# Performance work log

Measured on AMD Instinct MI355X. Metric: run time of the kernel, lower is better.

The kernel has to match this reference:

```python
import jax, jax.numpy as jnp
import numpy as np

N, D, V = 262144, 3, 64
CAPACITY = 1 << 20  # hash table size (number of lattice vertices storable)
PRIMES = np.array([2654435761, 805459861, 3674653429], dtype=np.uint32)


def setup_inputs() -> dict:
    key = jax.random.key(0)
    k1, k2 = jax.random.split(key)
    positions = jax.random.normal(k1, (N, D), dtype=jnp.float32) * 2.0
    values = jax.random.normal(k2, (N, V), dtype=jnp.float32)
    return {"positions": positions, "values": values}


def _splat(positions, values):
    """Permutohedral-lattice splat: scatter-add barycentric-weighted homogeneous
    values into a hashed lattice table of shape [CAPACITY, V+1]."""
    n, d = positions.shape
    dp1 = d + 1
    # elevation scale factors (standard permutohedral construction)
    inv_std = np.sqrt(2.0 / 3.0) * dp1
    scale = (inv_std / np.sqrt((np.arange(d) + 1.0) * (np.arange(d) + 2.0))).astype(np.float32)
    cf = positions * scale                                   # [N, d]
    # elevated[i] = sum_{j>=i} cf_j - i * cf_{i-1}
    suf = jnp.cumsum(cf[:, ::-1], axis=1)[:, ::-1]           # suffix sums [N, d]
    suf_ext = jnp.concatenate([suf, jnp.zeros((n, 1), cf.dtype)], axis=1)  # [N, d+1]
    cf_pad = jnp.concatenate([jnp.zeros((n, 1), cf.dtype), cf], axis=1)
    i_arr = jnp.arange(dp1, dtype=cf.dtype)
    elev = suf_ext - i_arr * cf_pad                           # [N, d+1]

    # nearest 0-colored remainder point
    rd = jnp.round(elev / dp1)
    rem0 = rd * dp1                                           # [N, d+1]
    rd_sum = jnp.sum(rd, axis=1).astype(jnp.int32)            # [N]

    # rank: sort order of (elev - rem0), ties broken by index
    diff = elev - rem0
    dj = diff[:, :, None]
    di = diff[:, None, :]
    jidx = jnp.arange(dp1)[:, None]
    iidx = jnp.arange(dp1)[None, :]
    rank = jnp.sum(((dj > di) | ((dj == di) & (jidx < iidx))).astype(jnp.int32), axis=1)
    rank = rank + rd_sum[:, None]
    under = rank < 0
    over = rank > d
    rank = rank + jnp.where(under, dp1, 0) - jnp.where(over, dp1, 0)
    rem0 = rem0 + (under.astype(cf.dtype) - over.astype(cf.dtype)) * dp1

    # barycentric weights (length d+2, last entry folded into bary[0])
    delta = (elev - rem0) / dp1                               # [N, d+1]
    oh = (jax.nn.one_hot(d - rank, d + 2, dtype=cf.dtype)
          - jax.nn.one_hot(d + 1 - rank, d + 2, dtype=cf.dtype))  # [N, d+1, d+2]
    bary = jnp.einsum('nik,ni->nk', oh, delta)
    bary = bary.at[:, 0].add(1.0 + bary[:, d + 1])
    w = bary[:, :dp1]                                         # [N, d+1] simplex weights

    # simplex vertex keys per remainder r (only first d coords needed)
    r_arr = jnp.arange(dp1, dtype=jnp.int32)                  # [d+1]
    r_b = r_arr[None, :, None]                                # [1, d+1, 1]
    offs = jnp.where(rank[:, None, :d] < dp1 - r_b, r_b, r_b - dp1)  # [N, d+1, d]
    keys = rem0[:, None, :d].astype(jnp.int32) + offs         # [N, d+1, d]

    # hash keys into table slots
    h = (keys.astype(jnp.uint32) * jnp.asarray(PRIMES)).sum(-1) % jnp.uint32(CAPACITY)
    h = h.astype(jnp.int32)                                   # [N, d+1]

    # scatter-add weighted homogeneous values
    vh = jnp.concatenate([values, jnp.ones((n, 1), values.dtype)], axis=1)  # [N, V+1]
    contrib = w[:, :, None] * vh[:, None, :]                  # [N, d+1, V+1]
    table = jnp.zeros((CAPACITY, vh.shape[1]), values.dtype)
    table = table.at[h.reshape(-1)].add(contrib.reshape(-1, vh.shape[1]))
    return table


def reference(positions, values):
    return _splat(positions, values)
```

## Files before the change

### kernel.cpp

```cpp
#include <hip/hip_runtime.h>
#include <stdint.h>


#define CAPACITY (1u << 20)
#define KCAP     (1u << 20)
#define TBL_W 65
#define CHUNK 64

__device__ __forceinline__ void lattice_all(const float* __restrict__ pos, int point,
                                            uint32_t h[4], float w[4], uint32_t* keyOut)
{
    const float scale0 = 2.3094010767585034f;
    const float scale1 = 1.3333333333333333f;
    const float scale2 = 0.9428090415820634f;

    const float cf0 = pos[point * 3 + 0] * scale0;
    const float cf1 = pos[point * 3 + 1] * scale1;
    const float cf2 = pos[point * 3 + 2] * scale2;

    const float t1 = cf2 + cf1;
    float elev[4];
    elev[0] = t1 + cf0;
    elev[1] = t1 - cf0;
    elev[2] = cf2 - 2.0f * cf1;
    elev[3] = -3.0f * cf2;

    float rem0[4];
    float rd_s = 0.0f;
#pragma unroll
    for (int j = 0; j < 4; ++j) {
        float rd = rintf(elev[j] * 0.25f);
        rem0[j] = rd * 4.0f;
        rd_s += rd;
    }
    const int rd_sum = (int)rd_s;

    float diff[4];
#pragma unroll
    for (int j = 0; j < 4; ++j) diff[j] = elev[j] - rem0[j];

    int rank[4];
#pragma unroll
    for (int i = 0; i < 4; ++i) {
        int r = 0;
#pragma unroll
        for (int j = 0; j < 4; ++j) {
            if (diff[j] > diff[i] || (diff[j] == diff[i] && j < i)) r++;
        }
        rank[i] = r + rd_sum;
    }

#pragma unroll
    for (int i = 0; i < 4; ++i) {
        if (rank[i] < 0)      { rank[i] += 4; rem0[i] += 4.0f; }
        else if (rank[i] > 3) { rank[i] -= 4; rem0[i] -= 4.0f; }
    }

    float delta[4];
#pragma unroll
    for (int i = 0; i < 4; ++i) delta[i] = (elev[i] - rem0[i]) * 0.25f;

    float b[5] = {0.f, 0.f, 0.f, 0.f, 0.f};
#pragma unroll
    for (int i = 0; i < 4; ++i) {
        int k1 = 3 - rank[i];
        int k2 = 4 - rank[i];
        if (k1 >= 0 && k1 < 5) b[k1] += delta[i];
        if (k2 >= 0 && k2 < 5) b[k2] -= delta[i];
    }
    w[0] = b[0] + (1.0f + b[4]);
    w[1] = b[1];
    w[2] = b[2];
    w[3] = b[3];

    const uint32_t P0 = 2654435761u, P1 = 805459861u, P2 = 3674653429u;
    const int k0  = (int)rem0[0];
    const int k1i = (int)rem0[1];
    const int k2i = (int)rem0[2];

#pragma unroll
    for (int r = 0; r < 4; ++r) {
        int o0 = (rank[0] < 4 - r) ? r : r - 4;
        int o1 = (rank[1] < 4 - r) ? r : r - 4;
        int o2 = (rank[2] < 4 - r) ? r : r - 4;
        uint32_t hh = (uint32_t)(k0 + o0)  * P0
                    + (uint32_t)(k1i + o1) * P1
                    + (uint32_t)(k2i + o2) * P2;
        h[r] = hh & (CAPACITY - 1u);
    }

    const uint32_t pidx = (uint32_t)(rank[0] * 16 + rank[1] * 4 + rank[2]);
    uint32_t key = (uint32_t)k0 * P0 + (uint32_t)k1i * P1 + (uint32_t)k2i * P2
                 + pidx * 0x9E3779B9u;
    *keyOut = key & (KCAP - 1u);
}

__global__ __launch_bounds__(256) void k_hist(const float* __restrict__ pos,
                                              uint32_t* __restrict__ counts,
                                              uint32_t* __restrict__ keys, int n)
{
    int p = blockIdx.x * blockDim.x + threadIdx.x;
    if (p >= n) return;
    uint32_t h[4]; float w[4]; uint32_t key;
    lattice_all(pos, p, h, w, &key);
    keys[p] = key;
    atomicAdd(&counts[key], 1u);
}

__global__ __launch_bounds__(256) void k_blocksum(const uint32_t* __restrict__ counts,
                                                  uint32_t* __restrict__ partials)
{
    __shared__ uint32_t s[256];
    const int b = blockIdx.x, t = threadIdx.x;
    uint4 v = ((const uint4*)(counts + (size_t)b * 1024))[t];
    s[t] = v.x + v.y + v.z + v.w;
    __syncthreads();
    for (int o = 128; o > 0; o >>= 1) {
        if (t < o) s[t] += s[t + o];
        __syncthreads();
    }
    if (t == 0) partials[b] = s[0];
}

__global__ __launch_bounds__(1024) void k_scanpartials(uint32_t* __restrict__ partials,
                                                       int npart)
{
    __shared__ uint32_t s[1024];
    const int t = threadIdx.x;
    const int k = npart >> 10;
    uint32_t v[8];
    uint32_t tot = 0;
    for (int j = 0; j < k; ++j) { v[j] = partials[t * k + j]; tot += v[j]; }
    s[t] = tot;
    __syncthreads();
    for (int o = 1; o < 1024; o <<= 1) {
        uint32_t x = s[t];
        uint32_t y = (t >= o) ? s[t - o] : 0u;
        __syncthreads();
        s[t] = x + y;
        __syncthreads();
    }
    uint32_t run = (t > 0) ? s[t - 1] : 0u;
    for (int j = 0; j < k; ++j) {
        uint32_t tmp = v[j];
        partials[t * k + j] = run;
        run += tmp;
    }
}

__global__ __launch_bounds__(256) void k_offsets(const uint32_t* __restrict__ counts,
                                                 const uint32_t* __restrict__ partials,
                                                 uint32_t* __restrict__ offsets)
{
    __shared__ uint32_t s[256];
    const int b = blockIdx.x, t = threadIdx.x;
    uint4 v = ((const uint4*)(counts + (size_t)b * 1024))[t];
    s[t] = v.x + v.y + v.z + v.w;
    __syncthreads();
    for (int o = 1; o < 256; o <<= 1) {
        uint32_t x = s[t];
        uint32_t y = (t >= o) ? s[t - o] : 0u;
        __syncthreads();
        s[t] = x + y;
        __syncthreads();
    }
    uint32_t texcl = ((t > 0) ? s[t - 1] : 0u) + partials[b];
    uint4 o4;
    o4.x = texcl;
    o4.y = texcl + v.x;
    o4.z = o4.y + v.y;
    o4.w = o4.z + v.z;
    ((uint4*)(offsets + (size_t)b * 1024))[t] = o4;
}

__global__ __launch_bounds__(256) void k_scatter(const uint32_t* __restrict__ keys,
                                                 const uint32_t* __restrict__ offsets,
                                                 uint32_t* __restrict__ counts,
                                                 uint32_t* __restrict__ sorted, int n)
{
    int p = blockIdx.x * blockDim.x + threadIdx.x;
    if (p >= n) return;
    const uint32_t key = keys[p];
    uint32_t slot = atomicSub(&counts[key], 1u) - 1u;
    sorted[offsets[key] + slot] = (uint32_t)p;
}

__global__ __launch_bounds__(256) void k_reduce(const uint32_t* __restrict__ sorted,
                                                const float* __restrict__ pos,
                                                const float* __restrict__ vals,
                                                float* __restrict__ table, int N)
{
    const int gtid = blockIdx.x * blockDim.x + threadIdx.x;
    const int wid  = gtid >> 6;
    const int lane = threadIdx.x & 63;
    const int base = wid * CHUNK;
    if (base >= N) return;
    const int cnt = min(CHUNK, N - base);

    const int e = (lane < cnt) ? lane : 0;
    const int mypid = (int)sorted[base + e];

    uint32_t mh[4]; float mw[4]; uint32_t dummyKey;
    lattice_all(pos, mypid, mh, mw, &dummyKey);

    uint32_t h0p = __shfl(mh[0], 0);
    uint32_t h1p = __shfl(mh[1], 0);
    uint32_t h2p = __shfl(mh[2], 0);
    uint32_t h3p = __shfl(mh[3], 0);

    float acc0 = 0.f, acc1 = 0.f, acc2 = 0.f, acc3 = 0.f;
    float aW0 = 0.f, aW1 = 0.f, aW2 = 0.f, aW3 = 0.f;

    for (int eb = 0; eb < cnt; eb += 8) {
        const int m = min(8, cnt - eb);
        float row[8];
#pragma unroll
        for (int j = 0; j < 8; ++j) {
            const int pj = __shfl(mypid, (eb + j) & (CHUNK - 1));
            row[j] = (j < m) ? vals[(size_t)pj * 64 + lane] : 0.f;
        }
#pragma unroll
        for (int j = 0; j < 8; ++j) {
            if (j >= m) break;
            const int src = eb + j;
            const uint32_t h0c = __shfl(mh[0], src);
            const uint32_t h1c = __shfl(mh[1], src);
            const uint32_t h2c = __shfl(mh[2], src);
            const uint32_t h3c = __shfl(mh[3], src);
            if ((h0c != h0p) | (h1c != h1p) | (h2c != h2p) | (h3c != h3p)) {
                atomicAdd(&table[(size_t)h0p * TBL_W + lane], acc0);
                atomicAdd(&table[(size_t)h1p * TBL_W + lane], acc1);
                atomicAdd(&table[(size_t)h2p * TBL_W + lane], acc2);
                atomicAdd(&table[(size_t)h3p * TBL_W + lane], acc3);
                if (lane == 0) {
                    atomicAdd(&table[(size_t)h0p * TBL_W + 64], aW0);
                    atomicAdd(&table[(size_t)h1p * TBL_W + 64], aW1);
                    atomicAdd(&table[(size_t)h2p * TBL_W + 64], aW2);
                    atomicAdd(&table[(size_t)h3p * TBL_W + 64], aW3);
                }
                acc0 = acc1 = acc2 = acc3 = 0.f;
                aW0 = aW1 = aW2 = aW3 = 0.f;
                h0p = h0c; h1p = h1c; h2p = h2c; h3p = h3c;
            }
            const float w0 = __shfl(mw[0], src);
            const float w1 = __shfl(mw[1], src);
            const float w2 = __shfl(mw[2], src);
            const float w3 = __shfl(mw[3], src);
            acc0 += w0 * row[j];
            acc1 += w1 * row[j];
            acc2 += w2 * row[j];
            acc3 += w3 * row[j];
            aW0 += w0; aW1 += w1; aW2 += w2; aW3 += w3;
        }
    }
    atomicAdd(&table[(size_t)h0p * TBL_W + lane], acc0);
    atomicAdd(&table[(size_t)h1p * TBL_W + lane], acc1);
    atomicAdd(&table[(size_t)h2p * TBL_W + lane], acc2);
    atomicAdd(&table[(size_t)h3p * TBL_W + lane], acc3);
    if (lane == 0) {
        atomicAdd(&table[(size_t)h0p * TBL_W + 64], aW0);
        atomicAdd(&table[(size_t)h1p * TBL_W + 64], aW1);
        atomicAdd(&table[(size_t)h2p * TBL_W + 64], aW2);
        atomicAdd(&table[(size_t)h3p * TBL_W + 64], aW3);
    }
}

__global__ __launch_bounds__(256) void splat_fallback(const float* __restrict__ pos,
                                                      const float* __restrict__ vals,
                                                      float* __restrict__ table, int n)
{
    const int gtid  = blockIdx.x * blockDim.x + threadIdx.x;
    const int point = gtid >> 6;
    const int lane  = threadIdx.x & 63;
    if (point >= n) return;
    uint32_t h[4]; float w[4]; uint32_t key;
    lattice_all(pos, point, h, w, &key);
    const float v = vals[(size_t)point * 64 + lane];
#pragma unroll
    for (int r = 0; r < 4; ++r)
        atomicAdd(&table[(size_t)h[r] * TBL_W + lane], w[r] * v);
    if (lane == 0) {
#pragma unroll
        for (int r = 0; r < 4; ++r)
            atomicAdd(&table[(size_t)h[r] * TBL_W + 64], w[r]);
    }
}

extern "C" void kernel_launch(void* const* d_in, const int* in_sizes, int n_in,
                              void* d_out, int out_size, void* d_ws, size_t ws_size,
                              hipStream_t stream) {
    const float* pos  = (const float*)d_in[0];
    const float* vals = (const float*)d_in[1];
    float* table      = (float*)d_out;

    const int n = in_sizes[0] / 3;

    hipMemsetAsync(d_out, 0, (size_t)out_size * sizeof(float), stream);

    const size_t SZ_CNT  = (size_t)KCAP * 4;
    const size_t offCnt  = 0;
    const size_t offOff  = offCnt + SZ_CNT;
    const size_t offPart = offOff + SZ_CNT;
    const size_t offKeys = offPart + 4096;
    const size_t offSort = offKeys + (size_t)n * 4;
    const size_t REQUIRED = offSort + (size_t)n * 4;

    if (ws_size < REQUIRED) {
        const int blocks = (n * 64 + 255) / 256;
        splat_fallback<<<blocks, 256, 0, stream>>>(pos, vals, table, n);
        return;
    }

    uint8_t* ws = (uint8_t*)d_ws;
    uint32_t* counts   = (uint32_t*)(ws + offCnt);
    uint32_t* offsets  = (uint32_t*)(ws + offOff);
    uint32_t* partials = (uint32_t*)(ws + offPart);
    uint32_t* keys     = (uint32_t*)(ws + offKeys);
    uint32_t* sorted   = (uint32_t*)(ws + offSort);

    hipMemsetAsync(counts, 0, SZ_CNT, stream);

    const int ptBlocks = (n + 255) / 256;
    k_hist<<<ptBlocks, 256, 0, stream>>>(pos, counts, keys, n);

    const int scanBlocks = KCAP / 1024;
    k_blocksum    <<<scanBlocks, 256,  0, stream>>>(counts, partials);
    k_scanpartials<<<1,          1024, 0, stream>>>(partials, scanBlocks);
    k_offsets     <<<scanBlocks, 256,  0, stream>>>(counts, partials, offsets);

    k_scatter<<<ptBlocks, 256, 0, stream>>>(keys, offsets, counts, sorted, n);

    const int nWaves  = (n + CHUNK - 1) / CHUNK;
    const int rBlocks = (nWaves + 3) / 4;
    k_reduce<<<rBlocks, 256, 0, stream>>>(sorted, pos, vals, table, n);
}
```

Before: 128.7 us.

## Shrink sort key space and fuse output zeroing into histogram kernel

Reduces the counting-sort key space from 2^20 to 2^18 buckets, so the counts memset, block sums, scan and offsets kernels touch a quarter of the data, and the partials scan becomes a single 256-thread pass. The separate memset of the large output table is removed and done instead by a grid-stride uint4 zeroing loop inside the histogram kernel, which now launches a fixed 2048 blocks. More key collisions from the smaller space only affect grouping locality, not correctness, and zeroing now competes with histogram atomics for bandwidth.

After: 148.1 us. 15.0% more time.

```diff
diff --git a/kernel.cpp b/kernel.cpp
--- a/kernel.cpp
+++ b/kernel.cpp
@@ -3,9 +3,9 @@
 
 
 #define CAPACITY (1u << 20)
-#define KCAP     (1u << 20)
-#define TBL_W 65
-#define CHUNK 64
+#define KCAP     (1u << 18)
+#define TBL_W    65
+#define CHUNK    64
 
 __device__ __forceinline__ void lattice_all(const float* __restrict__ pos, int point,
                                             uint32_t h[4], float w[4], uint32_t* keyOut)
@@ -95,16 +95,23 @@
     *keyOut = key & (KCAP - 1u);
 }
 
-__global__ __launch_bounds__(256) void k_hist(const float* __restrict__ pos,
-                                              uint32_t* __restrict__ counts,
-                                              uint32_t* __restrict__ keys, int n)
-{
-    int p = blockIdx.x * blockDim.x + threadIdx.x;
-    if (p >= n) return;
-    uint32_t h[4]; float w[4]; uint32_t key;
-    lattice_all(pos, p, h, w, &key);
-    keys[p] = key;
-    atomicAdd(&counts[key], 1u);
+__global__ __launch_bounds__(256) void k_hist_zero(const float* __restrict__ pos,
+                                                   uint32_t* __restrict__ counts,
+                                                   uint32_t* __restrict__ keys,
+                                                   uint4* __restrict__ table4,
+                                                   int n, int tbl4)
+{
+    const int gtid = blockIdx.x * blockDim.x + threadIdx.x;
+    const int nthreads = gridDim.x * blockDim.x;
+
+    if (gtid < n) {
+        uint32_t h[4]; float w[4]; uint32_t key;
+        lattice_all(pos, gtid, h, w, &key);
+        keys[gtid] = key;
+        atomicAdd(&counts[key], 1u);
+    }
+    const uint4 z = make_uint4(0u, 0u, 0u, 0u);
+    for (size_t i = (size_t)gtid; i < (size_t)tbl4; i += nthreads) table4[i] = z;
 }
 
 __global__ __launch_bounds__(256) void k_blocksum(const uint32_t* __restrict__ counts,
@@ -122,30 +129,21 @@
     if (t == 0) partials[b] = s[0];
 }
 
-__global__ __launch_bounds__(1024) void k_scanpartials(uint32_t* __restrict__ partials,
-                                                       int npart)
-{
-    __shared__ uint32_t s[1024];
+__global__ __launch_bounds__(256) void k_scanpart256(uint32_t* __restrict__ partials)
+{
+    __shared__ uint32_t s[256];
     const int t = threadIdx.x;
-    const int k = npart >> 10;
-    uint32_t v[8];
-    uint32_t tot = 0;
-    for (int j = 0; j < k; ++j) { v[j] = partials[t * k + j]; tot += v[j]; }
-    s[t] = tot;
+    const uint32_t v = partials[t];
+    s[t] = v;
     __syncthreads();
-    for (int o = 1; o < 1024; o <<= 1) {
+    for (int o = 1; o < 256; o <<= 1) {
         uint32_t x = s[t];
         uint32_t y = (t >= o) ? s[t - o] : 0u;
         __syncthreads();
         s[t] = x + y;
         __syncthreads();
     }
-    uint32_t run = (t > 0) ? s[t - 1] : 0u;
-    for (int j = 0; j < k; ++j) {
-        uint32_t tmp = v[j];
-        partials[t * k + j] = run;
-        run += tmp;
-    }
+    partials[t] = s[t] - v;
 }
 
 __global__ __launch_bounds__(256) void k_offsets(const uint32_t* __restrict__ counts,
@@ -164,7 +162,7 @@
         s[t] = x + y;
         __syncthreads();
     }
-    uint32_t texcl = ((t > 0) ? s[t - 1] : 0u) + partials[b];
+    uint32_t texcl = (s[t] - (v.x + v.y + v.z + v.w)) + partials[b];
     uint4 o4;
     o4.x = texcl;
     o4.y = texcl + v.x;
@@ -295,8 +293,6 @@
 
     const int n = in_sizes[0] / 3;
 
-    hipMemsetAsync(d_out, 0, (size_t)out_size * sizeof(float), stream);
-
     const size_t SZ_CNT  = (size_t)KCAP * 4;
     const size_t offCnt  = 0;
     const size_t offOff  = offCnt + SZ_CNT;
@@ -305,7 +301,8 @@
     const size_t offSort = offKeys + (size_t)n * 4;
     const size_t REQUIRED = offSort + (size_t)n * 4;
 
-    if (ws_size < REQUIRED) {
+    if (ws_size < REQUIRED || (out_size & 3)) {
+        hipMemsetAsync(d_out, 0, (size_t)out_size * sizeof(float), stream);
         const int blocks = (n * 64 + 255) / 256;
         splat_fallback<<<blocks, 256, 0, stream>>>(pos, vals, table, n);
         return;
@@ -320,14 +317,15 @@
 
     hipMemsetAsync(counts, 0, SZ_CNT, stream);
 
+    const int tbl4 = out_size / 4;
+    k_hist_zero<<<2048, 256, 0, stream>>>(pos, counts, keys, (uint4*)table, n, tbl4);
+
+    const int scanBlocks = KCAP / 1024;
+    k_blocksum   <<<scanBlocks, 256, 0, stream>>>(counts, partials);
+    k_scanpart256<<<1,          256, 0, stream>>>(partials);
+    k_offsets    <<<scanBlocks, 256, 0, stream>>>(counts, partials, offsets);
+
     const int ptBlocks = (n + 255) / 256;
-    k_hist<<<ptBlocks, 256, 0, stream>>>(pos, counts, keys, n);
-
-    const int scanBlocks = KCAP / 1024;
-    k_blocksum    <<<scanBlocks, 256,  0, stream>>>(counts, partials);
-    k_scanpartials<<<1,          1024, 0, stream>>>(partials, scanBlocks);
-    k_offsets     <<<scanBlocks, 256,  0, stream>>>(counts, partials, offsets);
-
     k_scatter<<<ptBlocks, 256, 0, stream>>>(keys, offsets, counts, sorted, n);
 
     const int nWaves  = (n + CHUNK - 1) / CHUNK;
```
